# Kernel tuning notes

Hardware: AMD Instinct MI355X
Metric: run time of the kernel (lower is better)

## Reference

```python
import jax, jax.numpy as jnp
import numpy as np

N = 4096
D = 256          # hidden_dim
H = 8            # num_heads
HD = D // H      # head_dim
EPS = 1e-5
SCALE = D ** -0.5  # note: full hidden_dim, as in the torch code


def setup_inputs() -> dict:
    key = jax.random.key(0)
    ks = jax.random.split(key, 12)
    # binary-ish adjacency mask in [0,1); zeros/near-zeros act like masked entries
    A = (jax.random.uniform(ks[0], (N, N)) < 0.01).astype(jnp.float32)
    h = jax.random.normal(ks[1], (N, D), dtype=jnp.float32)
    s = D ** -0.5
    Wq = jax.random.normal(ks[2], (D, D), dtype=jnp.float32) * s
    Wk = jax.random.normal(ks[3], (D, D), dtype=jnp.float32) * s
    Wv = jax.random.normal(ks[4], (D, D), dtype=jnp.float32) * s
    Wo = jax.random.normal(ks[5], (D, D), dtype=jnp.float32) * s
    g1 = jnp.ones((D,), jnp.float32)
    b1 = jnp.zeros((D,), jnp.float32)
    g2 = jnp.ones((D,), jnp.float32)
    b2 = jnp.zeros((D,), jnp.float32)
    W1 = jax.random.normal(ks[6], (2 * D, D), dtype=jnp.float32) * s
    W2 = jax.random.normal(ks[7], (D, 2 * D), dtype=jnp.float32) * (2 * D) ** -0.5
    return {"A": A, "h": h, "Wq": Wq, "Wk": Wk, "Wv": Wv, "Wo": Wo,
            "g1": g1, "b1": b1, "g2": g2, "b2": b2, "W1": W1, "W2": W2}


def _batchnorm(x, g, b):
    # training-mode BatchNorm1d over node/batch dim, biased variance
    m = x.mean(axis=0)
    v = x.var(axis=0)
    return (x - m) * jax.lax.rsqrt(v + EPS) * g + b


def _mha(A, h, Wq, Wk, Wv, Wo):
    # torch reshape(N, head_dim, num_heads): head index is the fastest axis
    q = (h @ Wq.T).reshape(N, HD, H) * SCALE   # [N, hd, H]
    k = (h @ Wk.T).reshape(N, HD, H)
    v = (h @ Wv.T).reshape(N, HD, H)
    scores = jnp.einsum('ndh,mdh->hnm', q, k)  # [H, N, N]
    attn = jax.nn.softmax(A[None, :, :] * scores, axis=2)
    out = jnp.einsum('hnm,mdh->ndh', attn, v)  # [N, hd, H]
    return out.reshape(N, D) @ Wo.T


def reference(A, h, Wq, Wk, Wv, Wo, g1, b1, g2, b2, W1, W2):
    h1 = h
    h = _mha(A, h, Wq, Wk, Wv, Wo)
    h = h + h1                       # residual
    h = _batchnorm(h, g1, b1)
    h2 = h
    h = jax.nn.relu(h @ W1.T) @ W2.T  # FFN (no bias)
    h = h2 + h                       # residual
    h = _batchnorm(h, g2, b2)
    return h
```

## Files before the change

### kernel.cpp

```cpp
#include <hip/hip_runtime.h>
#include <math.h>

#define NN 4096
#define DIM 256
#define NHEAD 8
#define HDIM 32
#define DFF 512
#define CAP 128
#define EPS_BN 1e-5f
#define QSCALE 0.0625f
#define MB (1u << 20)

typedef __attribute__((ext_vector_type(8))) short short8;
typedef __attribute__((ext_vector_type(4))) float f32x4;

__device__ inline ushort f2bf(float x) {
    unsigned u = __builtin_bit_cast(unsigned, x);
    unsigned r = u + 0x7FFF + ((u >> 16) & 1);
    return (ushort)(r >> 16);
}
__device__ inline float bf2f(ushort u) {
    return __builtin_bit_cast(float, (unsigned)u << 16);
}
__device__ inline float bflo(unsigned u) { return __builtin_bit_cast(float, u << 16); }
__device__ inline float bfhi(unsigned u) { return __builtin_bit_cast(float, u & 0xFFFF0000u); }

__global__ __launch_bounds__(256) void prep(
    const float* __restrict__ s0, const float* __restrict__ s1,
    const float* __restrict__ s2, const float* __restrict__ s3,
    const float* __restrict__ s4, const float* __restrict__ s5,
    const float* __restrict__ s6,
    ushort* d0, ushort* d1, ushort* d2, ushort* d3,
    ushort* d4, ushort* d5, ushort* d6,
    const float* __restrict__ A, int* __restrict__ idx,
    float* __restrict__ av, int* __restrict__ cnt)
{
    __shared__ int scan[256];
    int b = blockIdx.x, tid = threadIdx.x;
    if (b < 768) {
        const float* s; ushort* d; int off;
        if      (b < 512) { s = s0; d = d0; off = b; }
        else if (b < 544) { s = s1; d = d1; off = b - 512; }
        else if (b < 576) { s = s2; d = d2; off = b - 544; }
        else if (b < 608) { s = s3; d = d3; off = b - 576; }
        else if (b < 640) { s = s4; d = d4; off = b - 608; }
        else if (b < 704) { s = s5; d = d5; off = b - 640; }
        else              { s = s6; d = d6; off = b - 704; }
        size_t base = (size_t)off * 2048 + (size_t)tid * 8;
        float4 f0 = *(const float4*)(s + base);
        float4 f1 = *(const float4*)(s + base + 4);
        uint4 u;
        u.x = (unsigned)f2bf(f0.x) | ((unsigned)f2bf(f0.y) << 16);
        u.y = (unsigned)f2bf(f0.z) | ((unsigned)f2bf(f0.w) << 16);
        u.z = (unsigned)f2bf(f1.x) | ((unsigned)f2bf(f1.y) << 16);
        u.w = (unsigned)f2bf(f1.z) | ((unsigned)f2bf(f1.w) << 16);
        *(uint4*)(d + base) = u;
        return;
    }
    int n = b - 768;
    const float* row = A + (size_t)n * NN;
    float4 vals[4];
    int c = 0;
    #pragma unroll
    for (int i = 0; i < 4; ++i) {
        vals[i] = *(const float4*)(row + i * 1024 + tid * 4);
        c += (vals[i].x != 0.f) + (vals[i].y != 0.f)
           + (vals[i].z != 0.f) + (vals[i].w != 0.f);
    }
    scan[tid] = c;
    __syncthreads();
    for (int off = 1; off < 256; off <<= 1) {
        int t = (tid >= off) ? scan[tid - off] : 0;
        __syncthreads();
        scan[tid] += t;
        __syncthreads();
    }
    int pos = scan[tid] - c;
    int total = scan[255];
    #pragma unroll
    for (int i = 0; i < 4; ++i) {
        int cb = i * 1024 + tid * 4;
        float4 v = vals[i];
        if (v.x != 0.f && pos < CAP) { idx[n*CAP+pos] = cb;     av[n*CAP+pos] = v.x; ++pos; }
        if (v.y != 0.f && pos < CAP) { idx[n*CAP+pos] = cb + 1; av[n*CAP+pos] = v.y; ++pos; }
        if (v.z != 0.f && pos < CAP) { idx[n*CAP+pos] = cb + 2; av[n*CAP+pos] = v.z; ++pos; }
        if (v.w != 0.f && pos < CAP) { idx[n*CAP+pos] = cb + 3; av[n*CAP+pos] = v.w; ++pos; }
    }
    if (tid == 0) cnt[n] = min(total, CAP);
}

#define LDP 88
#define TSTRIDE 74
__global__ __launch_bounds__(256) void gemm_bf(
    const void* __restrict__ Aptr, const ushort* __restrict__ B,
    const float* __restrict__ scA, const float* __restrict__ shA,
    const float* __restrict__ resid,
    const float* yres, const float* __restrict__ scR, const float* __restrict__ shR,
    float* Cf, ushort* __restrict__ Cb,
    ushort* __restrict__ qh, ushort* __restrict__ kvh,
    float* __restrict__ bnps, float* __restrict__ bnpq,
    float* __restrict__ vpart,
    int M, int Nn, int K, int aMode, int storeMode, int relu, int bnstat)
{
    __shared__ ushort As[64][LDP];
    __shared__ ushort Bs[64][LDP];
    __shared__ float sRedS[8][64];
    __shared__ float sRedQ[8][64];
    int tid = threadIdx.x;
    int lane = tid & 63, w = tid >> 6;
    int wm = (w >> 1) * 32, wn = (w & 1) * 32;
    int nbx = gridDim.x, nbyq = gridDim.y >> 3;
    int orig = blockIdx.y * nbx + blockIdx.x;
    int xcd = orig & 7, pos = orig >> 3;
    int by = xcd * nbyq + pos / nbx;
    int bx = pos % nbx;
    int m0 = by * 64, n0 = bx * 64;
    int l15 = lane & 15, lk = lane >> 4;

    int srow = tid >> 3;
    int scol = (tid & 7) * 8;

    f32x4 acc[2][2] = {};
    for (int k0 = 0; k0 < K; k0 += 64) {
        uint4 ga0, ga1, gb0, gb1;
        const ushort* Bg = B + (size_t)(n0 + srow) * K + scol + k0;
        gb0 = *(const uint4*)Bg;
        gb1 = *(const uint4*)(Bg + (size_t)32 * K);
        if (aMode == 0) {
            const ushort* Ag = (const ushort*)Aptr + (size_t)(m0 + srow) * K + scol + k0;
            ga0 = *(const uint4*)Ag;
            ga1 = *(const uint4*)(Ag + (size_t)32 * K);
        } else {
            const float* Af = (const float*)Aptr + (size_t)(m0 + srow) * K + scol + k0;
            float4 sc0 = *(const float4*)(scA + k0 + scol);
            float4 sc1 = *(const float4*)(scA + k0 + scol + 4);
            float4 sh0 = *(const float4*)(shA + k0 + scol);
            float4 sh1 = *(const float4*)(shA + k0 + scol + 4);
            float4 a0 = *(const float4*)Af;
            float4 a1 = *(const float4*)(Af + 4);
            float4 b0 = *(const float4*)(Af + (size_t)32 * K);
            float4 b1 = *(const float4*)(Af + (size_t)32 * K + 4);
            ga0.x = (unsigned)f2bf(a0.x*sc0.x+sh0.x) | ((unsigned)f2bf(a0.y*sc0.y+sh0.y) << 16);
            ga0.y = (unsigned)f2bf(a0.z*sc0.z+sh0.z) | ((unsigned)f2bf(a0.w*sc0.w+sh0.w) << 16);
            ga0.z = (unsigned)f2bf(a1.x*sc1.x+sh1.x) | ((unsigned)f2bf(a1.y*sc1.y+sh1.y) << 16);
            ga0.w = (unsigned)f2bf(a1.z*sc1.z+sh1.z) | ((unsigned)f2bf(a1.w*sc1.w+sh1.w) << 16);
            ga1.x = (unsigned)f2bf(b0.x*sc0.x+sh0.x) | ((unsigned)f2bf(b0.y*sc0.y+sh0.y) << 16);
            ga1.y = (unsigned)f2bf(b0.z*sc0.z+sh0.z) | ((unsigned)f2bf(b0.w*sc0.w+sh0.w) << 16);
            ga1.z = (unsigned)f2bf(b1.x*sc1.x+sh1.x) | ((unsigned)f2bf(b1.y*sc1.y+sh1.y) << 16);
            ga1.w = (unsigned)f2bf(b1.z*sc1.z+sh1.z) | ((unsigned)f2bf(b1.w*sc1.w+sh1.w) << 16);
        }
        __syncthreads();
        *(uint4*)&As[srow][scol]      = ga0;
        *(uint4*)&As[srow + 32][scol] = ga1;
        *(uint4*)&Bs[srow][scol]      = gb0;
        *(uint4*)&Bs[srow + 32][scol] = gb1;
        __syncthreads();
        #pragma unroll
        for (int ks = 0; ks < 2; ++ks) {
            int kc = ks * 32 + lk * 8;
            short8 a0 = *(const short8*)&As[wm      + l15][kc];
            short8 a1 = *(const short8*)&As[wm + 16 + l15][kc];
            short8 b0 = *(const short8*)&Bs[wn      + l15][kc];
            short8 b1 = *(const short8*)&Bs[wn + 16 + l15][kc];
            acc[0][0] = __builtin_amdgcn_mfma_f32_16x16x32_bf16(a0, b0, acc[0][0], 0, 0, 0);
            acc[0][1] = __builtin_amdgcn_mfma_f32_16x16x32_bf16(a0, b1, acc[0][1], 0, 0, 0);
            acc[1][0] = __builtin_amdgcn_mfma_f32_16x16x32_bf16(a1, b0, acc[1][0], 0, 0, 0);
            acc[1][1] = __builtin_amdgcn_mfma_f32_16x16x32_bf16(a1, b1, acc[1][1], 0, 0, 0);
        }
    }

    if (storeMode == 2) {
        ushort* sT = &As[0][0];
        int seg = n0 >> 8, ddBase = (n0 & 255) >> 3;
        float sp[2] = {0.f, 0.f};
        __syncthreads();
        #pragma unroll
        for (int mt = 0; mt < 2; ++mt)
            #pragma unroll
            for (int nt = 0; nt < 2; ++nt) {
                int col_l = wn + nt * 16 + l15;
                #pragma unroll
                for (int i = 0; i < 4; ++i) {
                    int row_l = wm + mt * 16 + lk * 4 + i;
                    float v = acc[mt][nt][i];
                    if (seg == 0) v *= QSCALE;
                    sT[row_l * TSTRIDE + col_l] = f2bf(v);
                    sp[nt] += v;
                }
            }
        __syncthreads();
        for (int c = tid; c < 512; c += 256) {
            int rl = c & 63, hh = c >> 6;
            const ushort* tp = sT + rl * TSTRIDE + hh;
            uint4 pk;
            pk.x = (unsigned)tp[0]  | ((unsigned)tp[8]  << 16);
            pk.y = (unsigned)tp[16] | ((unsigned)tp[24] << 16);
            pk.z = (unsigned)tp[32] | ((unsigned)tp[40] << 16);
            pk.w = (unsigned)tp[48] | ((unsigned)tp[56] << 16);
            int row = m0 + rl;
            if (seg == 0)
                *(uint4*)(qh + ((size_t)hh * NN + row) * HDIM + ddBase) = pk;
            else
                *(uint4*)(kvh + ((size_t)hh * NN + row) * 64 +
                          ((seg == 2) ? 32 : 0) + ddBase) = pk;
        }
        if (seg == 2) {
            int slot = ((wm >> 5) << 2) | lk;
            sRedS[slot][wn + l15]      = sp[0];
            sRedS[slot][wn + 16 + l15] = sp[1];
            __syncthreads();
            if (tid < 64) {
                float ss = 0.f;
                #pragma unroll
                for (int r = 0; r < 8; ++r) ss += sRedS[r][tid];
                vpart[(size_t)by * 256 + (n0 & 255) + tid] = ss;
            }
        }
        return;
    }

    float sp[2] = {0.f, 0.f}, qp[2] = {0.f, 0.f};
    #pragma unroll
    for (int mt = 0; mt < 2; ++mt) {
        #pragma unroll
        for (int nt = 0; nt < 2; ++nt) {
            int col = n0 + wn + nt * 16 + l15;
            #pragma unroll
            for (int i = 0; i < 4; ++i) {
                int row = m0 + wm + mt * 16 + lk * 4 + i;
                float v = acc[mt][nt][i];
                if (storeMode == 0) {
                    if (resid) v += resid[(size_t)row * Nn + col];
                    Cf[(size_t)row * Nn + col] = v;
                } else if (storeMode == 1) {
                    if (relu) v = fmaxf(v, 0.f);
                    Cb[(size_t)row * Nn + col] = f2bf(v);
                } else {
                    v += yres[(size_t)row * Nn + col] * scR[col] + shR[col];
                    Cf[(size_t)row * Nn + col] = v;
                }
                if (bnstat) { sp[nt] += v; qp[nt] += v * v; }
            }
        }
    }
    if (bnstat) {
        int slot = ((wm >> 5) << 2) | lk;
        sRedS[slot][wn + l15]      = sp[0];
        sRedQ[slot][wn + l15]      = qp[0];
        sRedS[slot][wn + 16 + l15] = sp[1];
        sRedQ[slot][wn + 16 + l15] = qp[1];
        __syncthreads();
        if (tid < 64) {
            float ss = 0.f, qq = 0.f;
            #pragma unroll
            for (int r = 0; r < 8; ++r) { ss += sRedS[r][tid]; qq += sRedQ[r][tid]; }
            bnps[(size_t)by * DIM + n0 + tid] = ss;
            bnpq[(size_t)by * DIM + n0 + tid] = qq;
        }
    }
}

__global__ __launch_bounds__(256) void vsum_final(
    const float* __restrict__ vpart, float* __restrict__ vsumh)
{
    int c = threadIdx.x;
    float s = 0.f;
    #pragma unroll 8
    for (int b = 0; b < 64; ++b) s += vpart[(size_t)b * 256 + c];
    vsumh[(c & 7) * HDIM + (c >> 3)] = s;
}

__global__ __launch_bounds__(1024) void colreduce_final2(
    const float* __restrict__ ps, const float* __restrict__ pq,
    const float* __restrict__ g, const float* __restrict__ bsh,
    float* __restrict__ scale, float* __restrict__ shift)
{
    __shared__ float rs_[4][256], rq_[4][256];
    int t = threadIdx.x;
    int c = t & 255, qd = t >> 8;
    float s = 0.f, q = 0.f;
    for (int b = qd; b < 64; b += 4) {
        s += ps[b * DIM + c];
        q += pq[b * DIM + c];
    }
    rs_[qd][c] = s; rq_[qd][c] = q;
    __syncthreads();
    if (qd == 0) {
        s = rs_[0][c] + rs_[1][c] + rs_[2][c] + rs_[3][c];
        q = rq_[0][c] + rq_[1][c] + rq_[2][c] + rq_[3][c];
        float m = s * (1.f / NN);
        float var = q * (1.f / NN) - m * m;
        float rstd = rsqrtf(var + EPS_BN);
        float sc = rstd * g[c];
        scale[c] = sc;
        shift[c] = bsh[c] - m * sc;
    }
}

__global__ __launch_bounds__(256) void bn_apply_fin(
    const float* __restrict__ x, const float* __restrict__ scale,
    const float* __restrict__ shift, float* __restrict__ out)
{
    int tid = threadIdx.x;
    size_t i = (size_t)blockIdx.x * 1024 + (size_t)tid * 4;
    int c = (tid * 4) & 255;
    float4 v = *(const float4*)(x + i);
    float4 sc = *(const float4*)(scale + c);
    float4 sh = *(const float4*)(shift + c);
    float4 r;
    r.x = v.x * sc.x + sh.x;
    r.y = v.y * sc.y + sh.y;
    r.z = v.z * sc.z + sh.z;
    r.w = v.w * sc.w + sh.w;
    *(float4*)(out + i) = r;
}

__global__ __launch_bounds__(256) void attn2(
    const ushort* __restrict__ qh, const ushort* __restrict__ kvh,
    const float* __restrict__ vsumh,
    const int* __restrict__ idx, const float* __restrict__ av,
    const int* __restrict__ cnt, ushort* __restrict__ out)
{
    __shared__ float sQ[NHEAD][HDIM];
    __shared__ int   sIdx[CAP];
    __shared__ float sAv[CAP];
    __shared__ float sS[CAP][NHEAD];
    __shared__ float red[32][NHEAD];
    __shared__ float sRd[NHEAD];
    __shared__ float4 sO[4][64];

    int tid = threadIdx.x, n = blockIdx.x;
    int nnz = cnt[n];
    {
        int h = tid >> 5, d = tid & 31;
        sQ[h][d] = bf2f(qh[((size_t)h * NN + n) * HDIM + d]);
    }
    if (tid < nnz) {
        sIdx[tid] = idx[n * CAP + tid];
        sAv[tid]  = av[n * CAP + tid];
    }
    __syncthreads();

    int h8 = tid & 7, jr = tid >> 3;
    float4 qreg[8];
    #pragma unroll
    for (int t = 0; t < 8; ++t) qreg[t] = ((const float4*)sQ[h8])[t];
    float lsum = 0.0f;
    for (int jb = 0; jb < nnz; jb += 32) {
        int j = jb + jr;
        if (j < nnz) {
            int m = sIdx[j];
            const uint4* kp = (const uint4*)(kvh + ((size_t)h8 * NN + m) * 64);
            uint4 k0 = kp[0], k1 = kp[1], k2 = kp[2], k3 = kp[3];
            float s =
                bflo(k0.x)*qreg[0].x + bfhi(k0.x)*qreg[0].y +
                bflo(k0.y)*qreg[0].z + bfhi(k0.y)*qreg[0].w +
                bflo(k0.z)*qreg[1].x + bfhi(k0.z)*qreg[1].y +
                bflo(k0.w)*qreg[1].z + bfhi(k0.w)*qreg[1].w +
                bflo(k1.x)*qreg[2].x + bfhi(k1.x)*qreg[2].y +
                bflo(k1.y)*qreg[2].z + bfhi(k1.y)*qreg[2].w +
                bflo(k1.z)*qreg[3].x + bfhi(k1.z)*qreg[3].y +
                bflo(k1.w)*qreg[3].z + bfhi(k1.w)*qreg[3].w +
                bflo(k2.x)*qreg[4].x + bfhi(k2.x)*qreg[4].y +
                bflo(k2.y)*qreg[4].z + bfhi(k2.y)*qreg[4].w +
                bflo(k2.z)*qreg[5].x + bfhi(k2.z)*qreg[5].y +
                bflo(k2.w)*qreg[5].z + bfhi(k2.w)*qreg[5].w +
                bflo(k3.x)*qreg[6].x + bfhi(k3.x)*qreg[6].y +
                bflo(k3.y)*qreg[6].z + bfhi(k3.y)*qreg[6].w +
                bflo(k3.z)*qreg[7].x + bfhi(k3.z)*qreg[7].y +
                bflo(k3.w)*qreg[7].z + bfhi(k3.w)*qreg[7].w;
            s *= sAv[j];
            float ww = __expf(s);
            sS[j][h8] = ww - 1.0f;
            lsum += ww;
        }
    }
    red[jr][h8] = lsum;
    __syncthreads();
    if (jr < 16) red[jr][h8] += red[jr + 16][h8];
    __syncthreads();
    if (jr < 8)  red[jr][h8] += red[jr + 8][h8];
    __syncthreads();
    if (jr < 4)  red[jr][h8] += red[jr + 4][h8];
    __syncthreads();
    if (jr < 2)  red[jr][h8] += red[jr + 2][h8];
    __syncthreads();
    if (jr == 0) {
        float den = red[0][h8] + red[1][h8] + (float)(NN - nnz);
        sRd[h8] = 1.0f / den;
    }
    __syncthreads();

    int wv = tid >> 6, lane = tid & 63;
    int h3 = lane >> 3, dq = lane & 7;
    float a0 = 0.f, a1 = 0.f, a2 = 0.f, a3 = 0.f;
    const ushort* vbase = kvh + (size_t)h3 * NN * 64 + 32 + dq * 4;
    for (int j = wv; j < nnz; j += 4) {
        float ww = sS[j][h3];
        uint2 vv = *(const uint2*)(vbase + (size_t)sIdx[j] * 64);
        a0 += ww * bflo(vv.x); a1 += ww * bfhi(vv.x);
        a2 += ww * bflo(vv.y); a3 += ww * bfhi(vv.y);
    }
    sO[wv][lane] = make_float4(a0, a1, a2, a3);
    __syncthreads();
    if (tid < 64) {
        int h = tid >> 3, dq2 = tid & 7;
        float4 p0 = sO[0][tid], p1 = sO[1][tid], p2 = sO[2][tid], p3 = sO[3][tid];
        float rd = sRd[h];
        int d0 = dq2 * 4;
        float r0 = (p0.x + p1.x + p2.x + p3.x + vsumh[h * HDIM + d0 + 0]) * rd;
        float r1 = (p0.y + p1.y + p2.y + p3.y + vsumh[h * HDIM + d0 + 1]) * rd;
        float r2 = (p0.z + p1.z + p2.z + p3.z + vsumh[h * HDIM + d0 + 2]) * rd;
        float r3 = (p0.w + p1.w + p2.w + p3.w + vsumh[h * HDIM + d0 + 3]) * rd;
        size_t ob = (size_t)n * DIM + h;
        out[ob + (d0 + 0) * 8] = f2bf(r0);
        out[ob + (d0 + 1) * 8] = f2bf(r1);
        out[ob + (d0 + 2) * 8] = f2bf(r2);
        out[ob + (d0 + 3) * 8] = f2bf(r3);
    }
}

extern "C" void kernel_launch(void* const* d_in, const int* in_sizes, int n_in,
                              void* d_out, int out_size, void* d_ws, size_t ws_size,
                              hipStream_t stream)
{
    const float* A  = (const float*)d_in[0];
    const float* h  = (const float*)d_in[1];
    const float* Wq = (const float*)d_in[2];
    const float* Wk = (const float*)d_in[3];
    const float* Wv = (const float*)d_in[4];
    const float* Wo = (const float*)d_in[5];
    const float* g1 = (const float*)d_in[6];
    const float* b1 = (const float*)d_in[7];
    const float* g2 = (const float*)d_in[8];
    const float* b2 = (const float*)d_in[9];
    const float* W1 = (const float*)d_in[10];
    const float* W2 = (const float*)d_in[11];
    float* out = (float*)d_out;
    char* w = (char*)d_ws;

    int*    nzidx  = (int*)(w);
    float*  nzav   = (float*)(w + 2 * MB);
    int*    nzcnt  = (int*)(w + 4 * MB);
    ushort* h_bf   = (ushort*)(w + 5 * MB);
    ushort* wqkv   = (ushort*)(w + 7 * MB);
    ushort* wo_b   = (ushort*)(w + 7 * MB + 384 * 1024);
    ushort* w1_b   = (ushort*)(w + 7 * MB + 512 * 1024);
    ushort* w2_b   = (ushort*)(w + 7 * MB + 768 * 1024);
    ushort* qh_bf  = (ushort*)(w + 8 * MB);
    ushort* kvh    = (ushort*)(w + 10 * MB);
    ushort* ao_bf  = (ushort*)(w + 14 * MB);
    float*  y      = (float*)(w + 16 * MB);
    ushort* t_bf   = (ushort*)(w + 20 * MB);
    float*  vpart  = (float*)(w + 24 * MB);
    float*  bnps   = (float*)(w + 25 * MB);
    float*  bnpq   = (float*)(w + 25 * MB + 64 * 1024);
    float*  scale1 = (float*)(w + 26 * MB);
    float*  shift1 = scale1 + 256;
    float*  scale2 = scale1 + 512;
    float*  shift2 = scale1 + 768;
    float*  vsumh  = scale1 + 1024;

    dim3 blk(256);

    prep<<<4864, blk, 0, stream>>>(h, Wq, Wk, Wv, Wo, W1, W2,
        h_bf, wqkv, wqkv + 65536, wqkv + 131072, wo_b, w1_b, w2_b,
        A, nzidx, nzav, nzcnt);
    gemm_bf<<<dim3(12, 64), blk, 0, stream>>>(h_bf, wqkv,
        nullptr, nullptr, nullptr, nullptr, nullptr, nullptr,
        nullptr, nullptr, qh_bf, kvh, nullptr, nullptr, vpart,
        NN, 768, DIM, 0, 2, 0, 0);
    vsum_final<<<1, blk, 0, stream>>>(vpart, vsumh);
    attn2<<<NN, blk, 0, stream>>>(qh_bf, kvh, vsumh, nzidx, nzav, nzcnt, ao_bf);
    gemm_bf<<<dim3(4, 64), blk, 0, stream>>>(ao_bf, wo_b,
        nullptr, nullptr, h, nullptr, nullptr, nullptr,
        y, nullptr, nullptr, nullptr, bnps, bnpq, nullptr,
        NN, DIM, DIM, 0, 0, 0, 1);
    colreduce_final2<<<1, dim3(1024), 0, stream>>>(bnps, bnpq, g1, b1, scale1, shift1);
    gemm_bf<<<dim3(8, 64), blk, 0, stream>>>(y, w1_b,
        scale1, shift1, nullptr, nullptr, nullptr, nullptr,
        nullptr, t_bf, nullptr, nullptr, nullptr, nullptr, nullptr,
        NN, DFF, DIM, 1, 1, 1, 0);
    gemm_bf<<<dim3(4, 64), blk, 0, stream>>>(t_bf, w2_b,
        nullptr, nullptr, nullptr, y, scale1, shift1,
        y, nullptr, nullptr, nullptr, bnps, bnpq, nullptr,
        NN, DIM, DFF, 0, 3, 0, 1);
    colreduce_final2<<<1, dim3(1024), 0, stream>>>(bnps, bnpq, g2, b2, scale2, shift2);
    bn_apply_fin<<<1024, blk, 0, stream>>>(y, scale2, shift2, out);
}
```

Before: 95.13 us.

## Fuse adjacency scan into QKV GEMM and remap attention to head-per-block

```diff
diff --git a/kernel.cpp b/kernel.cpp
--- a/kernel.cpp
+++ b/kernel.cpp
@@ -25,81 +25,175 @@
 __device__ inline float bflo(unsigned u) { return __builtin_bit_cast(float, u << 16); }
 __device__ inline float bfhi(unsigned u) { return __builtin_bit_cast(float, u & 0xFFFF0000u); }
 
-__global__ __launch_bounds__(256) void prep(
+__global__ __launch_bounds__(256) void convert_bf(
     const float* __restrict__ s0, const float* __restrict__ s1,
     const float* __restrict__ s2, const float* __restrict__ s3,
     const float* __restrict__ s4, const float* __restrict__ s5,
     const float* __restrict__ s6,
     ushort* d0, ushort* d1, ushort* d2, ushort* d3,
-    ushort* d4, ushort* d5, ushort* d6,
-    const float* __restrict__ A, int* __restrict__ idx,
-    float* __restrict__ av, int* __restrict__ cnt)
-{
-    __shared__ int scan[256];
+    ushort* d4, ushort* d5, ushort* d6)
+{
     int b = blockIdx.x, tid = threadIdx.x;
-    if (b < 768) {
-        const float* s; ushort* d; int off;
-        if      (b < 512) { s = s0; d = d0; off = b; }
-        else if (b < 544) { s = s1; d = d1; off = b - 512; }
-        else if (b < 576) { s = s2; d = d2; off = b - 544; }
-        else if (b < 608) { s = s3; d = d3; off = b - 576; }
-        else if (b < 640) { s = s4; d = d4; off = b - 608; }
-        else if (b < 704) { s = s5; d = d5; off = b - 640; }
-        else              { s = s6; d = d6; off = b - 704; }
-        size_t base = (size_t)off * 2048 + (size_t)tid * 8;
-        float4 f0 = *(const float4*)(s + base);
-        float4 f1 = *(const float4*)(s + base + 4);
-        uint4 u;
-        u.x = (unsigned)f2bf(f0.x) | ((unsigned)f2bf(f0.y) << 16);
-        u.y = (unsigned)f2bf(f0.z) | ((unsigned)f2bf(f0.w) << 16);
-        u.z = (unsigned)f2bf(f1.x) | ((unsigned)f2bf(f1.y) << 16);
-        u.w = (unsigned)f2bf(f1.z) | ((unsigned)f2bf(f1.w) << 16);
-        *(uint4*)(d + base) = u;
-        return;
-    }
-    int n = b - 768;
-    const float* row = A + (size_t)n * NN;
-    float4 vals[4];
-    int c = 0;
-    #pragma unroll
-    for (int i = 0; i < 4; ++i) {
-        vals[i] = *(const float4*)(row + i * 1024 + tid * 4);
-        c += (vals[i].x != 0.f) + (vals[i].y != 0.f)
-           + (vals[i].z != 0.f) + (vals[i].w != 0.f);
-    }
-    scan[tid] = c;
-    __syncthreads();
-    for (int off = 1; off < 256; off <<= 1) {
-        int t = (tid >= off) ? scan[tid - off] : 0;
-        __syncthreads();
-        scan[tid] += t;
-        __syncthreads();
-    }
-    int pos = scan[tid] - c;
-    int total = scan[255];
-    #pragma unroll
-    for (int i = 0; i < 4; ++i) {
-        int cb = i * 1024 + tid * 4;
-        float4 v = vals[i];
-        if (v.x != 0.f && pos < CAP) { idx[n*CAP+pos] = cb;     av[n*CAP+pos] = v.x; ++pos; }
-        if (v.y != 0.f && pos < CAP) { idx[n*CAP+pos] = cb + 1; av[n*CAP+pos] = v.y; ++pos; }
-        if (v.z != 0.f && pos < CAP) { idx[n*CAP+pos] = cb + 2; av[n*CAP+pos] = v.z; ++pos; }
-        if (v.w != 0.f && pos < CAP) { idx[n*CAP+pos] = cb + 3; av[n*CAP+pos] = v.w; ++pos; }
-    }
-    if (tid == 0) cnt[n] = min(total, CAP);
+    const float* s; ushort* d; int off;
+    if      (b < 512) { s = s0; d = d0; off = b; }
+    else if (b < 544) { s = s1; d = d1; off = b - 512; }
+    else if (b < 576) { s = s2; d = d2; off = b - 544; }
+    else if (b < 608) { s = s3; d = d3; off = b - 576; }
+    else if (b < 640) { s = s4; d = d4; off = b - 608; }
+    else if (b < 704) { s = s5; d = d5; off = b - 640; }
+    else              { s = s6; d = d6; off = b - 704; }
+    size_t base = (size_t)off * 2048 + (size_t)tid * 8;
+    float4 f0 = *(const float4*)(s + base);
+    float4 f1 = *(const float4*)(s + base + 4);
+    uint4 u;
+    u.x = (unsigned)f2bf(f0.x) | ((unsigned)f2bf(f0.y) << 16);
+    u.y = (unsigned)f2bf(f0.z) | ((unsigned)f2bf(f0.w) << 16);
+    u.z = (unsigned)f2bf(f1.x) | ((unsigned)f2bf(f1.y) << 16);
+    u.w = (unsigned)f2bf(f1.z) | ((unsigned)f2bf(f1.w) << 16);
+    *(uint4*)(d + base) = u;
 }
 
 #define LDP 88
 #define TSTRIDE 74
+__global__ __launch_bounds__(256) void qkv_ascan(
+    const ushort* __restrict__ Ah, const ushort* __restrict__ B,
+    ushort* __restrict__ qh, ushort* __restrict__ kvh,
+    float* __restrict__ vpart,
+    const float* __restrict__ Araw, unsigned* __restrict__ packed,
+    int* __restrict__ cnt)
+{
+    __shared__ ushort As[64][LDP];
+    __shared__ ushort Bs[64][LDP];
+    __shared__ float sRedS[8][64];
+    int b = blockIdx.x, tid = threadIdx.x;
+
+    if (b >= 768) {
+        int* scan = (int*)&As[0][0];
+        int n = b - 768;
+        const float* row = Araw + (size_t)n * NN;
+        float4 vals[4];
+        int c = 0;
+        #pragma unroll
+        for (int i = 0; i < 4; ++i) {
+            vals[i] = *(const float4*)(row + i * 1024 + tid * 4);
+            c += (vals[i].x != 0.f) + (vals[i].y != 0.f)
+               + (vals[i].z != 0.f) + (vals[i].w != 0.f);
+        }
+        scan[tid] = c;
+        __syncthreads();
+        for (int off = 1; off < 256; off <<= 1) {
+            int t = (tid >= off) ? scan[tid - off] : 0;
+            __syncthreads();
+            scan[tid] += t;
+            __syncthreads();
+        }
+        int pos = scan[tid] - c;
+        int total = scan[255];
+        #pragma unroll
+        for (int i = 0; i < 4; ++i) {
+            int cb = i * 1024 + tid * 4;
+            float4 v = vals[i];
+            if (v.x != 0.f && pos < CAP) { packed[n*CAP+pos] = ((unsigned)f2bf(v.x) << 16) | (unsigned)cb;       ++pos; }
+            if (v.y != 0.f && pos < CAP) { packed[n*CAP+pos] = ((unsigned)f2bf(v.y) << 16) | (unsigned)(cb + 1); ++pos; }
+            if (v.z != 0.f && pos < CAP) { packed[n*CAP+pos] = ((unsigned)f2bf(v.z) << 16) | (unsigned)(cb + 2); ++pos; }
+            if (v.w != 0.f && pos < CAP) { packed[n*CAP+pos] = ((unsigned)f2bf(v.w) << 16) | (unsigned)(cb + 3); ++pos; }
+        }
+        if (tid == 0) cnt[n] = min(total, CAP);
+        return;
+    }
+
+    int lane = tid & 63, w = tid >> 6;
+    int wm = (w >> 1) * 32, wn = (w & 1) * 32;
+    int xcd = b & 7, pos = b >> 3;
+    int by = xcd * 8 + pos / 12;
+    int bx = pos % 12;
+    int m0 = by * 64, n0 = bx * 64;
+    int l15 = lane & 15, lk = lane >> 4;
+    int srow = tid >> 3;
+    int scol = (tid & 7) * 8;
+
+    f32x4 acc[2][2] = {};
+    for (int k0 = 0; k0 < DIM; k0 += 64) {
+        const ushort* Bg = B + (size_t)(n0 + srow) * DIM + scol + k0;
+        uint4 gb0 = *(const uint4*)Bg;
+        uint4 gb1 = *(const uint4*)(Bg + (size_t)32 * DIM);
+        const ushort* Ag = Ah + (size_t)(m0 + srow) * DIM + scol + k0;
+        uint4 ga0 = *(const uint4*)Ag;
+        uint4 ga1 = *(const uint4*)(Ag + (size_t)32 * DIM);
+        __syncthreads();
+        *(uint4*)&As[srow][scol]      = ga0;
+        *(uint4*)&As[srow + 32][scol] = ga1;
+        *(uint4*)&Bs[srow][scol]      = gb0;
+        *(uint4*)&Bs[srow + 32][scol] = gb1;
+        __syncthreads();
+        #pragma unroll
+        for (int ks = 0; ks < 2; ++ks) {
+            int kc = ks * 32 + lk * 8;
+            short8 a0 = *(const short8*)&As[wm      + l15][kc];
+            short8 a1 = *(const short8*)&As[wm + 16 + l15][kc];
+            short8 b0 = *(const short8*)&Bs[wn      + l15][kc];
+            short8 b1 = *(const short8*)&Bs[wn + 16 + l15][kc];
+            acc[0][0] = __builtin_amdgcn_mfma_f32_16x16x32_bf16(a0, b0, acc[0][0], 0, 0, 0);
+            acc[0][1] = __builtin_amdgcn_mfma_f32_16x16x32_bf16(a0, b1, acc[0][1], 0, 0, 0);
+            acc[1][0] = __builtin_amdgcn_mfma_f32_16x16x32_bf16(a1, b0, acc[1][0], 0, 0, 0);
+            acc[1][1] = __builtin_amdgcn_mfma_f32_16x16x32_bf16(a1, b1, acc[1][1], 0, 0, 0);
+        }
+    }
+    ushort* sT = &As[0][0];
+    int seg = n0 >> 8, ddBase = (n0 & 255) >> 3;
+    float sp[2] = {0.f, 0.f};
+    __syncthreads();
+    #pragma unroll
+    for (int mt = 0; mt < 2; ++mt)
+        #pragma unroll
+        for (int nt = 0; nt < 2; ++nt) {
+            int col_l = wn + nt * 16 + l15;
+            #pragma unroll
+            for (int i = 0; i < 4; ++i) {
+                int row_l = wm + mt * 16 + lk * 4 + i;
+                float v = acc[mt][nt][i];
+                if (seg == 0) v *= QSCALE;
+                sT[row_l * TSTRIDE + col_l] = f2bf(v);
+                sp[nt] += v;
+            }
+        }
+    __syncthreads();
+    for (int c = tid; c < 512; c += 256) {
+        int rl = c & 63, hh = c >> 6;
+        const ushort* tp = sT + rl * TSTRIDE + hh;
+        uint4 pk;
+        pk.x = (unsigned)tp[0]  | ((unsigned)tp[8]  << 16);
+        pk.y = (unsigned)tp[16] | ((unsigned)tp[24] << 16);
+        pk.z = (unsigned)tp[32] | ((unsigned)tp[40] << 16);
+        pk.w = (unsigned)tp[48] | ((unsigned)tp[56] << 16);
+        int row = m0 + rl;
+        if (seg == 0)
+            *(uint4*)(qh + ((size_t)hh * NN + row) * HDIM + ddBase) = pk;
+        else
+            *(uint4*)(kvh + ((size_t)hh * NN + row) * 64 +
+                      ((seg == 2) ? 32 : 0) + ddBase) = pk;
+    }
+    if (seg == 2) {
+        int slot = ((wm >> 5) << 2) | lk;
+        sRedS[slot][wn + l15]      = sp[0];
+        sRedS[slot][wn + 16 + l15] = sp[1];
+        __syncthreads();
+        if (tid < 64) {
+            float ss = 0.f;
+            #pragma unroll
+            for (int r = 0; r < 8; ++r) ss += sRedS[r][tid];
+            vpart[(size_t)by * 256 + (n0 & 255) + tid] = ss;
+        }
+    }
+}
+
 __global__ __launch_bounds__(256) void gemm_bf(
     const void* __restrict__ Aptr, const ushort* __restrict__ B,
     const float* __restrict__ scA, const float* __restrict__ shA,
     const float* __restrict__ resid,
     const float* yres, const float* __restrict__ scR, const float* __restrict__ shR,
     float* Cf, ushort* __restrict__ Cb,
-    ushort* __restrict__ qh, ushort* __restrict__ kvh,
     float* __restrict__ bnps, float* __restrict__ bnpq,
-    float* __restrict__ vpart,
     int M, int Nn, int K, int aMode, int storeMode, int relu, int bnstat)
 {
     __shared__ ushort As[64][LDP];
@@ -116,7 +210,6 @@
     int bx = pos % nbx;
     int m0 = by * 64, n0 = bx * 64;
     int l15 = lane & 15, lk = lane >> 4;
-
     int srow = tid >> 3;
     int scol = (tid & 7) * 8;
 
@@ -169,56 +262,6 @@
         }
     }
 
-    if (storeMode == 2) {
-        ushort* sT = &As[0][0];
-        int seg = n0 >> 8, ddBase = (n0 & 255) >> 3;
-        float sp[2] = {0.f, 0.f};
-        __syncthreads();
-        #pragma unroll
-        for (int mt = 0; mt < 2; ++mt)
-            #pragma unroll
-            for (int nt = 0; nt < 2; ++nt) {
-                int col_l = wn + nt * 16 + l15;
-                #pragma unroll
-                for (int i = 0; i < 4; ++i) {
-                    int row_l = wm + mt * 16 + lk * 4 + i;
-                    float v = acc[mt][nt][i];
-                    if (seg == 0) v *= QSCALE;
-                    sT[row_l * TSTRIDE + col_l] = f2bf(v);
-                    sp[nt] += v;
-                }
-            }
-        __syncthreads();
-        for (int c = tid; c < 512; c += 256) {
-            int rl = c & 63, hh = c >> 6;
-            const ushort* tp = sT + rl * TSTRIDE + hh;
-            uint4 pk;
-            pk.x = (unsigned)tp[0]  | ((unsigned)tp[8]  << 16);
-            pk.y = (unsigned)tp[16] | ((unsigned)tp[24] << 16);
-            pk.z = (unsigned)tp[32] | ((unsigned)tp[40] << 16);
-            pk.w = (unsigned)tp[48] | ((unsigned)tp[56] << 16);
-            int row = m0 + rl;
-            if (seg == 0)
-                *(uint4*)(qh + ((size_t)hh * NN + row) * HDIM + ddBase) = pk;
-            else
-                *(uint4*)(kvh + ((size_t)hh * NN + row) * 64 +
-                          ((seg == 2) ? 32 : 0) + ddBase) = pk;
-        }
-        if (seg == 2) {
-            int slot = ((wm >> 5) << 2) | lk;
-            sRedS[slot][wn + l15]      = sp[0];
-            sRedS[slot][wn + 16 + l15] = sp[1];
-            __syncthreads();
-            if (tid < 64) {
-                float ss = 0.f;
-                #pragma unroll
-                for (int r = 0; r < 8; ++r) ss += sRedS[r][tid];
-                vpart[(size_t)by * 256 + (n0 & 255) + tid] = ss;
-            }
-        }
-        return;
-    }
-
     float sp[2] = {0.f, 0.f}, qp[2] = {0.f, 0.f};
     #pragma unroll
     for (int mt = 0; mt < 2; ++mt) {
@@ -315,109 +358,73 @@
     *(float4*)(out + i) = r;
 }
 
-__global__ __launch_bounds__(256) void attn2(
+__global__ __launch_bounds__(256) void attn3(
     const ushort* __restrict__ qh, const ushort* __restrict__ kvh,
     const float* __restrict__ vsumh,
-    const int* __restrict__ idx, const float* __restrict__ av,
-    const int* __restrict__ cnt, ushort* __restrict__ out)
-{
-    __shared__ float sQ[NHEAD][HDIM];
-    __shared__ int   sIdx[CAP];
-    __shared__ float sAv[CAP];
-    __shared__ float sS[CAP][NHEAD];
-    __shared__ float red[32][NHEAD];
-    __shared__ float sRd[NHEAD];
-    __shared__ float4 sO[4][64];
-
-    int tid = threadIdx.x, n = blockIdx.x;
+    const unsigned* __restrict__ packed, const int* __restrict__ cnt,
+    ushort* __restrict__ out)
+{
+    __shared__ float    sQ[8][32];
+    __shared__ unsigned sPk[8][CAP];
+    __shared__ float    sS[8][CAP];
+    __shared__ float    sRd[8];
+
+    int tid = threadIdx.x, b = blockIdx.x;
+    int hH = b & 7, rg = b >> 3;
+    int r = tid >> 5, l = tid & 31;
+    int n = rg * 8 + r;
     int nnz = cnt[n];
-    {
-        int h = tid >> 5, d = tid & 31;
-        sQ[h][d] = bf2f(qh[((size_t)h * NN + n) * HDIM + d]);
-    }
-    if (tid < nnz) {
-        sIdx[tid] = idx[n * CAP + tid];
-        sAv[tid]  = av[n * CAP + tid];
-    }
+
+    sQ[r][l] = bf2f(qh[((size_t)hH * NN + n) * HDIM + l]);
+    for (int j = l; j < nnz; j += 32) sPk[r][j] = packed[n * CAP + j];
     __syncthreads();
 
-    int h8 = tid & 7, jr = tid >> 3;
     float4 qreg[8];
     #pragma unroll
-    for (int t = 0; t < 8; ++t) qreg[t] = ((const float4*)sQ[h8])[t];
+    for (int t = 0; t < 8; ++t) qreg[t] = ((const float4*)sQ[r])[t];
     float lsum = 0.0f;
-    for (int jb = 0; jb < nnz; jb += 32) {
-        int j = jb + jr;
-        if (j < nnz) {
-            int m = sIdx[j];
-            const uint4* kp = (const uint4*)(kvh + ((size_t)h8 * NN + m) * 64);
-            uint4 k0 = kp[0], k1 = kp[1], k2 = kp[2], k3 = kp[3];
-            float s =
-                bflo(k0.x)*qreg[0].x + bfhi(k0.x)*qreg[0].y +
-                bflo(k0.y)*qreg[0].z + bfhi(k0.y)*qreg[0].w +
-                bflo(k0.z)*qreg[1].x + bfhi(k0.z)*qreg[1].y +
-                bflo(k0.w)*qreg[1].z + bfhi(k0.w)*qreg[1].w +
-                bflo(k1.x)*qreg[2].x + bfhi(k1.x)*qreg[2].y +
-                bflo(k1.y)*qreg[2].z + bfhi(k1.y)*qreg[2].w +
-                bflo(k1.z)*qreg[3].x + bfhi(k1.z)*qreg[3].y +
-                bflo(k1.w)*qreg[3].z + bfhi(k1.w)*qreg[3].w +
-                bflo(k2.x)*qreg[4].x + bfhi(k2.x)*qreg[4].y +
-                bflo(k2.y)*qreg[4].z + bfhi(k2.y)*qreg[4].w +
-                bflo(k2.z)*qreg[5].x + bfhi(k2.z)*qreg[5].y +
-                bflo(k2.w)*qreg[5].z + bfhi(k2.w)*qreg[5].w +
-                bflo(k3.x)*qreg[6].x + bfhi(k3.x)*qreg[6].y +
-                bflo(k3.y)*qreg[6].z + bfhi(k3.y)*qreg[6].w +
-                bflo(k3.z)*qreg[7].x + bfhi(k3.z)*qreg[7].y +
-                bflo(k3.w)*qreg[7].z + bfhi(k3.w)*qreg[7].w;
-            s *= sAv[j];
-            float ww = __expf(s);
-            sS[j][h8] = ww - 1.0f;
-            lsum += ww;
-        }
-    }
-    red[jr][h8] = lsum;
+    for (int j = l; j < nnz; j += 32) {
+        unsigned pk = sPk[r][j];
+        int m = pk & 0xFFFF;
+        float a = bfhi(pk);
+        const uint4* kp = (const uint4*)(kvh + ((size_t)hH * NN + m) * 64);
+        uint4 k0 = kp[0], k1 = kp[1], k2 = kp[2], k3 = kp[3];
+        float s =
+            bflo(k0.x)*qreg[0].x + bfhi(k0.x)*qreg[0].y +
+            bflo(k0.y)*qreg[0].z + bfhi(k0.y)*qreg[0].w +
+            bflo(k0.z)*qreg[1].x + bfhi(k0.z)*qreg[1].y +
+            bflo(k0.w)*qreg[1].z + bfhi(k0.w)*qreg[1].w +
+            bflo(k1.x)*qreg[2].x + bfhi(k1.x)*qreg[2].y +
+            bflo(k1.y)*qreg[2].z + bfhi(k1.y)*qreg[2].w +
+            bflo(k1.z)*qreg[3].x + bfhi(k1.z)*qreg[3].y +
+            bflo(k1.w)*qreg[3].z + bfhi(k1.w)*qreg[3].w +
+            bflo(k2.x)*qreg[4].x + bfhi(k2.x)*qreg[4].y +
+            bflo(k2.y)*qreg[4].z + bfhi(k2.y)*qreg[4].w +
+            bflo(k2.z)*qreg[5].x + bfhi(k2.z)*qreg[5].y +
+            bflo(k2.w)*qreg[5].z + bfhi(k2.w)*qreg[5].w +
+            bflo(k3.x)*qreg[6].x + bfhi(k3.x)*qreg[6].y +
+            bflo(k3.y)*qreg[6].z + bfhi(k3.y)*qreg[6].w +
+            bflo(k3.z)*qreg[7].x + bfhi(k3.z)*qreg[7].y +
+            bflo(k3.w)*qreg[7].z + bfhi(k3.w)*qreg[7].w;
+        s *= a;
+        float ww = __expf(s);
+        sS[r][j] = ww - 1.0f;
+        lsum += ww;
+    }
+    #pragma unroll
+    for (int o = 16; o > 0; o >>= 1) lsum += __shfl_xor(lsum, o, 32);
+    if (l == 0) sRd[r] = 1.0f / (lsum + (float)(NN - nnz));
     __syncthreads();
-    if (jr < 16) red[jr][h8] += red[jr + 16][h8];
-    __syncthreads();
-    if (jr < 8)  red[jr][h8] += red[jr + 8][h8];
-    __syncthreads();
-    if (jr < 4)  red[jr][h8] += red[jr + 4][h8];
-    __syncthreads();
-    if (jr < 2)  red[jr][h8] += red[jr + 2][h8];
-    __syncthreads();
-    if (jr == 0) {
-        float den = red[0][h8] + red[1][h8] + (float)(NN - nnz);
-        sRd[h8] = 1.0f / den;
-    }
-    __syncthreads();
-
-    int wv = tid >> 6, lane = tid & 63;
-    int h3 = lane >> 3, dq = lane & 7;
-    float a0 = 0.f, a1 = 0.f, a2 = 0.f, a3 = 0.f;
-    const ushort* vbase = kvh + (size_t)h3 * NN * 64 + 32 + dq * 4;
-    for (int j = wv; j < nnz; j += 4) {
-        float ww = sS[j][h3];
-        uint2 vv = *(const uint2*)(vbase + (size_t)sIdx[j] * 64);
-        a0 += ww * bflo(vv.x); a1 += ww * bfhi(vv.x);
-        a2 += ww * bflo(vv.y); a3 += ww * bfhi(vv.y);
-    }
-    sO[wv][lane] = make_float4(a0, a1, a2, a3);
-    __syncthreads();
-    if (tid < 64) {
-        int h = tid >> 3, dq2 = tid & 7;
-        float4 p0 = sO[0][tid], p1 = sO[1][tid], p2 = sO[2][tid], p3 = sO[3][tid];
-        float rd = sRd[h];
-        int d0 = dq2 * 4;
-        float r0 = (p0.x + p1.x + p2.x + p3.x + vsumh[h * HDIM + d0 + 0]) * rd;
-        float r1 = (p0.y + p1.y + p2.y + p3.y + vsumh[h * HDIM + d0 + 1]) * rd;
-        float r2 = (p0.z + p1.z + p2.z + p3.z + vsumh[h * HDIM + d0 + 2]) * rd;
-        float r3 = (p0.w + p1.w + p2.w + p3.w + vsumh[h * HDIM + d0 + 3]) * rd;
-        size_t ob = (size_t)n * DIM + h;
-        out[ob + (d0 + 0) * 8] = f2bf(r0);
-        out[ob + (d0 + 1) * 8] = f2bf(r1);
-        out[ob + (d0 + 2) * 8] = f2bf(r2);
-        out[ob + (d0 + 3) * 8] = f2bf(r3);
-    }
+
+    const ushort* vbase = kvh + (size_t)hH * NN * 64 + 32 + l;
+    float acc = 0.f;
+    #pragma unroll 4
+    for (int j = 0; j < nnz; ++j) {
+        int m = sPk[r][j] & 0xFFFF;
+        acc += sS[r][j] * bf2f(vbase[(size_t)m * 64]);
+    }
+    float res = (acc + vsumh[hH * HDIM + l]) * sRd[r];
+    out[(size_t)n * DIM + l * 8 + hH] = f2bf(res);
 }
 
 extern "C" void kernel_launch(void* const* d_in, const int* in_sizes, int n_in,
@@ -439,23 +446,22 @@
     float* out = (float*)d_out;
     char* w = (char*)d_ws;
 
-    int*    nzidx  = (int*)(w);
-    float*  nzav   = (float*)(w + 2 * MB);
-    int*    nzcnt  = (int*)(w + 4 * MB);
-    ushort* h_bf   = (ushort*)(w + 5 * MB);
-    ushort* wqkv   = (ushort*)(w + 7 * MB);
-    ushort* wo_b   = (ushort*)(w + 7 * MB + 384 * 1024);
-    ushort* w1_b   = (ushort*)(w + 7 * MB + 512 * 1024);
-    ushort* w2_b   = (ushort*)(w + 7 * MB + 768 * 1024);
-    ushort* qh_bf  = (ushort*)(w + 8 * MB);
-    ushort* kvh    = (ushort*)(w + 10 * MB);
-    ushort* ao_bf  = (ushort*)(w + 14 * MB);
-    float*  y      = (float*)(w + 16 * MB);
-    ushort* t_bf   = (ushort*)(w + 20 * MB);
-    float*  vpart  = (float*)(w + 24 * MB);
-    float*  bnps   = (float*)(w + 25 * MB);
-    float*  bnpq   = (float*)(w + 25 * MB + 64 * 1024);
-    float*  scale1 = (float*)(w + 26 * MB);
+    unsigned* packed = (unsigned*)(w);
+    int*    nzcnt  = (int*)(w + 2 * MB);
+    ushort* h_bf   = (ushort*)(w + 3 * MB);
+    ushort* wqkv   = (ushort*)(w + 5 * MB);
+    ushort* wo_b   = (ushort*)(w + 5 * MB + 384 * 1024);
+    ushort* w1_b   = (ushort*)(w + 5 * MB + 512 * 1024);
+    ushort* w2_b   = (ushort*)(w + 5 * MB + 768 * 1024);
+    ushort* qh_bf  = (ushort*)(w + 6 * MB);
+    ushort* kvh    = (ushort*)(w + 8 * MB);
+    ushort* ao_bf  = (ushort*)(w + 12 * MB);
+    float*  y      = (float*)(w + 14 * MB);
+    ushort* t_bf   = (ushort*)(w + 18 * MB);
+    float*  vpart  = (float*)(w + 22 * MB);
+    float*  bnps   = (float*)(w + 23 * MB);
+    float*  bnpq   = (float*)(w + 23 * MB + 64 * 1024);
+    float*  scale1 = (float*)(w + 24 * MB);
     float*  shift1 = scale1 + 256;
     float*  scale2 = scale1 + 512;
     float*  shift2 = scale1 + 768;
@@ -463,28 +469,22 @@
 
     dim3 blk(256);
 
-    prep<<<4864, blk, 0, stream>>>(h, Wq, Wk, Wv, Wo, W1, W2,
-        h_bf, wqkv, wqkv + 65536, wqkv + 131072, wo_b, w1_b, w2_b,
-        A, nzidx, nzav, nzcnt);
-    gemm_bf<<<dim3(12, 64), blk, 0, stream>>>(h_bf, wqkv,
-        nullptr, nullptr, nullptr, nullptr, nullptr, nullptr,
-        nullptr, nullptr, qh_bf, kvh, nullptr, nullptr, vpart,
-        NN, 768, DIM, 0, 2, 0, 0);
+    convert_bf<<<768, blk, 0, stream>>>(h, Wq, Wk, Wv, Wo, W1, W2,
+        h_bf, wqkv, wqkv + 65536, wqkv + 131072, wo_b, w1_b, w2_b);
+    qkv_ascan<<<4864, blk, 0, stream>>>(h_bf, wqkv, qh_bf, kvh, vpart,
+                                        A, packed, nzcnt);
     vsum_final<<<1, blk, 0, stream>>>(vpart, vsumh);
-    attn2<<<NN, blk, 0, stream>>>(qh_bf, kvh, vsumh, nzidx, nzav, nzcnt, ao_bf);
+    attn3<<<NN, blk, 0, stream>>>(qh_bf, kvh, vsumh, packed, nzcnt, ao_bf);
     gemm_bf<<<dim3(4, 64), blk, 0, stream>>>(ao_bf, wo_b,
         nullptr, nullptr, h, nullptr, nullptr, nullptr,
-        y, nullptr, nullptr, nullptr, bnps, bnpq, nullptr,
-        NN, DIM, DIM, 0, 0, 0, 1);
+        y, nullptr, bnps, bnpq, NN, DIM, DIM, 0, 0, 0, 1);
     colreduce_final2<<<1, dim3(1024), 0, stream>>>(bnps, bnpq, g1, b1, scale1, shift1);
     gemm_bf<<<dim3(8, 64), blk, 0, stream>>>(y, w1_b,
         scale1, shift1, nullptr, nullptr, nullptr, nullptr,
-        nullptr, t_bf, nullptr, nullptr, nullptr, nullptr, nullptr,
-        NN, DFF, DIM, 1, 1, 1, 0);
+        nullptr, t_bf, nullptr, nullptr, NN, DFF, DIM, 1, 1, 1, 0);
     gemm_bf<<<dim3(4, 64), blk, 0, stream>>>(t_bf, w2_b,
         nullptr, nullptr, nullptr, y, scale1, shift1,
-        y, nullptr, nullptr, nullptr, bnps, bnpq, nullptr,
-        NN, DIM, DFF, 0, 3, 0, 1);
+        y, nullptr, bnps, bnpq, NN, DIM, DFF, 0, 3, 0, 1);
     colreduce_final2<<<1, dim3(1024), 0, stream>>>(bnps, bnpq, g2, b2, scale2, shift2);
     bn_apply_fin<<<1024, blk, 0, stream>>>(y, scale2, shift2, out);
 }
```

After: 100.3 us. 1.05x slower.
